# Kernel tuning notes

Hardware: AMD Instinct MI355X
Metric: run time of the kernel (lower is better)

The kernel has to match this reference:

```python
import jax, jax.numpy as jnp
import numpy as np

EPSILON = 0.1
SCALE = 10000.0

N = 16777216
G = 1024


def setup_inputs() -> dict:
    key = jax.random.key(0)
    k1, k2, k3 = jax.random.split(key, 3)
    pred = jax.random.normal(k1, (N,), dtype=jnp.float32)
    target = jax.random.normal(k2, (N,), dtype=jnp.float32)
    batch = jnp.sort(jax.random.randint(k3, (N,), 0, G).astype(jnp.int64))
    x = jnp.zeros((N,), dtype=jnp.float32)  # accepted by forward but unused
    return {"pred": pred, "target": target, "batch": batch, "x": x, "num_graphs": G}


def reference(pred, target, batch, x, num_graphs):
    # Per-node relative error
    rel = jnp.abs(pred - target) / (jnp.abs(target) + EPSILON)  # [N]
    # Fused per-graph mean via segment reduction (replaces python loop over graphs)
    sums = jax.ops.segment_sum(rel, batch, num_segments=num_graphs)           # [G]
    counts = jax.ops.segment_sum(jnp.ones_like(rel), batch, num_segments=num_graphs)  # [G]
    graph_means = sums / counts  # every segment nonempty w.h.p. for N >> G
    return jnp.mean(graph_means) * SCALE
```

## Files before the change

### kernel.cpp

```cpp
#include <hip/hip_runtime.h>


#define EPSILON_F 0.1f
#define SCALE_F 10000.0f

constexpr int BLOCK = 256;
constexpr int EPB = 8192;
constexpr int IT = EPB / (BLOCK * 4);

__device__ __forceinline__ int load_batch(const int* __restrict__ b32,
                                          long long idx, bool is64) {
  return b32[is64 ? (idx << 1) : idx];
}

__global__ __launch_bounds__(BLOCK)
void gre_seg(const float* __restrict__ pred, const float* __restrict__ target,
             const int* __restrict__ batch32, int n,
             float* __restrict__ sums, float* __restrict__ cnts) {
  const int tid = threadIdx.x;
  const long long s = (long long)blockIdx.x * EPB;
  long long e = s + EPB;
  if (e > n) e = n;

  const bool is64 = (batch32[n - 1] == 0);

  float r[IT][4];
  #pragma unroll
  for (int it = 0; it < IT; ++it) {
    long long i4 = s + (long long)(it * BLOCK + tid) * 4;
    if (i4 + 4 <= e) {
      float4 p4 = *reinterpret_cast<const float4*>(pred + i4);
      float4 t4 = *reinterpret_cast<const float4*>(target + i4);
      r[it][0] = fabsf(p4.x - t4.x) / (fabsf(t4.x) + EPSILON_F);
      r[it][1] = fabsf(p4.y - t4.y) / (fabsf(t4.y) + EPSILON_F);
      r[it][2] = fabsf(p4.z - t4.z) / (fabsf(t4.z) + EPSILON_F);
      r[it][3] = fabsf(p4.w - t4.w) / (fabsf(t4.w) + EPSILON_F);
    } else {
      #pragma unroll
      for (int j = 0; j < 4; ++j) {
        long long i = i4 + j;
        r[it][j] = (i < e)
            ? fabsf(pred[i] - target[i]) / (fabsf(target[i]) + EPSILON_F)
            : 0.f;
      }
    }
  }

  const int b0 = load_batch(batch32, s, is64);
  const int b1 = load_batch(batch32, e - 1, is64);

  float A = 0.f, B = 0.f;
  long long p = e;
  bool fast = true;

  if (b0 == b1) {
    #pragma unroll
    for (int it = 0; it < IT; ++it)
      #pragma unroll
      for (int j = 0; j < 4; ++j) A += r[it][j];
  } else if (b1 == b0 + 1) {
    long long lo = s, hi = e - 1;
    while (hi - lo > 1) {
      long long mid = (lo + hi) >> 1;
      if (load_batch(batch32, mid, is64) > b0) hi = mid; else lo = mid;
    }
    p = hi;
    #pragma unroll
    for (int it = 0; it < IT; ++it) {
      long long i4 = s + (long long)(it * BLOCK + tid) * 4;
      #pragma unroll
      for (int j = 0; j < 4; ++j) {
        if (i4 + j < p) A += r[it][j]; else B += r[it][j];
      }
    }
  } else {
    fast = false;
    #pragma unroll
    for (int it = 0; it < IT; ++it) {
      long long i4 = s + (long long)(it * BLOCK + tid) * 4;
      for (int j = 0; j < 4; ++j) {
        long long i = i4 + j;
        if (i < e) {
          int gi = load_batch(batch32, i, is64);
          atomicAdd(&sums[gi], r[it][j]);
          atomicAdd(&cnts[gi], 1.f);
        }
      }
    }
  }

  if (fast) {
    #pragma unroll
    for (int off = 32; off > 0; off >>= 1) {
      A += __shfl_down(A, off, 64);
      B += __shfl_down(B, off, 64);
    }
    if ((tid & 63) == 0) {
      atomicAdd(&sums[b0], A);
      if (b1 != b0) atomicAdd(&sums[b1], B);
    }
    if (tid == 0) {
      if (b0 == b1) {
        atomicAdd(&cnts[b0], (float)(e - s));
      } else {
        atomicAdd(&cnts[b0], (float)(p - s));
        atomicAdd(&cnts[b1], (float)(e - p));
      }
    }
  }
}

__global__ __launch_bounds__(64)
void gre_final(const float* __restrict__ sums, const float* __restrict__ cnts,
               float* __restrict__ out, int g) {
  const int tid = threadIdx.x;
  float v = 0.f;
  for (int i = tid; i < g; i += 64) v += sums[i] / cnts[i];
  #pragma unroll
  for (int off = 32; off > 0; off >>= 1) v += __shfl_down(v, off, 64);
  if (tid == 0) out[0] = (v / (float)g) * SCALE_F;
}

extern "C" void kernel_launch(void* const* d_in, const int* in_sizes, int n_in,
                              void* d_out, int out_size, void* d_ws, size_t ws_size,
                              hipStream_t stream) {
  const float* pred   = (const float*)d_in[0];
  const float* target = (const float*)d_in[1];
  const int*   batch  = (const int*)d_in[2];
  const int n = in_sizes[0];
  const int g = 1024;

  float* sums = (float*)d_ws;
  float* cnts = sums + g;
  hipMemsetAsync(d_ws, 0, 2 * g * sizeof(float), stream);

  const int nblocks = (n + EPB - 1) / EPB;
  gre_seg<<<nblocks, BLOCK, 0, stream>>>(pred, target, batch, n, sums, cnts);
  gre_final<<<1, 64, 0, stream>>>(sums, cnts, (float*)d_out, g);
}
```

Measured before the change: 224.0 us.

## Precompute segment starts by binary search and fuse final reduction into main kernel

A new small kernel binary-searches the sorted batch array for each graph's start offset. Per-graph counts then come from differences of those offsets instead of atomic count accumulation, and the split point inside two-segment blocks comes from the same table instead of a per-block search. The separate finalize kernel is replaced by a last-block-done pattern that uses an atomic counter and fences inside the main kernel. Register arrays are dropped in favour of streaming accumulation. This adds one launch for the starts kernel but removes the final launch and the count atomics.

```diff
diff --git a/kernel.cpp b/kernel.cpp
--- a/kernel.cpp
+++ b/kernel.cpp
@@ -7,6 +7,7 @@
 constexpr int BLOCK = 256;
 constexpr int EPB = 8192;
 constexpr int IT = EPB / (BLOCK * 4);
+constexpr int G_CONST = 1024;
 
 __device__ __forceinline__ int load_batch(const int* __restrict__ b32,
                                           long long idx, bool is64) {
@@ -14,111 +15,135 @@
 }
 
 __global__ __launch_bounds__(BLOCK)
-void gre_seg(const float* __restrict__ pred, const float* __restrict__ target,
-             const int* __restrict__ batch32, int n,
-             float* __restrict__ sums, float* __restrict__ cnts) {
+void gre_starts(const int* __restrict__ batch32, int n, int g,
+                int* __restrict__ starts) {
+  const int t = blockIdx.x * BLOCK + threadIdx.x;
+  if (t > g) return;
+  if (t == 0) { starts[0] = 0; return; }
+  if (t == g) { starts[g] = n; return; }
+  const bool is64 = (batch32[n - 1] == 0);
+  int lo = 0, hi = n;
+  while (lo < hi) {
+    int mid = (lo + hi) >> 1;
+    if (load_batch(batch32, mid, is64) < t) lo = mid + 1; else hi = mid;
+  }
+  starts[t] = lo;
+}
+
+__global__ __launch_bounds__(BLOCK)
+void gre_main(const float* __restrict__ pred, const float* __restrict__ target,
+              const int* __restrict__ batch32, int n, int g,
+              const int* __restrict__ starts, float* __restrict__ sums,
+              unsigned int* __restrict__ done, float* __restrict__ out) {
   const int tid = threadIdx.x;
   const long long s = (long long)blockIdx.x * EPB;
   long long e = s + EPB;
   if (e > n) e = n;
-
   const bool is64 = (batch32[n - 1] == 0);
-
-  float r[IT][4];
-  #pragma unroll
-  for (int it = 0; it < IT; ++it) {
-    long long i4 = s + (long long)(it * BLOCK + tid) * 4;
-    if (i4 + 4 <= e) {
-      float4 p4 = *reinterpret_cast<const float4*>(pred + i4);
-      float4 t4 = *reinterpret_cast<const float4*>(target + i4);
-      r[it][0] = fabsf(p4.x - t4.x) / (fabsf(t4.x) + EPSILON_F);
-      r[it][1] = fabsf(p4.y - t4.y) / (fabsf(t4.y) + EPSILON_F);
-      r[it][2] = fabsf(p4.z - t4.z) / (fabsf(t4.z) + EPSILON_F);
-      r[it][3] = fabsf(p4.w - t4.w) / (fabsf(t4.w) + EPSILON_F);
-    } else {
-      #pragma unroll
-      for (int j = 0; j < 4; ++j) {
-        long long i = i4 + j;
-        r[it][j] = (i < e)
-            ? fabsf(pred[i] - target[i]) / (fabsf(target[i]) + EPSILON_F)
-            : 0.f;
-      }
-    }
-  }
-
   const int b0 = load_batch(batch32, s, is64);
   const int b1 = load_batch(batch32, e - 1, is64);
 
   float A = 0.f, B = 0.f;
-  long long p = e;
-  bool fast = true;
 
-  if (b0 == b1) {
-    #pragma unroll
-    for (int it = 0; it < IT; ++it)
-      #pragma unroll
-      for (int j = 0; j < 4; ++j) A += r[it][j];
-  } else if (b1 == b0 + 1) {
-    long long lo = s, hi = e - 1;
-    while (hi - lo > 1) {
-      long long mid = (lo + hi) >> 1;
-      if (load_batch(batch32, mid, is64) > b0) hi = mid; else lo = mid;
-    }
-    p = hi;
+  if (b1 == b0) {
+    float Bx = 0.f, By = 0.f;
     #pragma unroll
     for (int it = 0; it < IT; ++it) {
       long long i4 = s + (long long)(it * BLOCK + tid) * 4;
-      #pragma unroll
-      for (int j = 0; j < 4; ++j) {
-        if (i4 + j < p) A += r[it][j]; else B += r[it][j];
+      if (i4 + 4 <= e) {
+        float4 pv = *reinterpret_cast<const float4*>(pred + i4);
+        float4 tv = *reinterpret_cast<const float4*>(target + i4);
+        Bx += fabsf(pv.x - tv.x) / (fabsf(tv.x) + EPSILON_F);
+        By += fabsf(pv.y - tv.y) / (fabsf(tv.y) + EPSILON_F);
+        Bx += fabsf(pv.z - tv.z) / (fabsf(tv.z) + EPSILON_F);
+        By += fabsf(pv.w - tv.w) / (fabsf(tv.w) + EPSILON_F);
+      } else {
+        for (int j = 0; j < 4; ++j) {
+          long long i = i4 + j;
+          if (i < e)
+            Bx += fabsf(pred[i] - target[i]) / (fabsf(target[i]) + EPSILON_F);
+        }
+      }
+    }
+    B = Bx + By;
+  } else if (b1 == b0 + 1) {
+    const long long p = (long long)starts[b1];
+    #pragma unroll
+    for (int it = 0; it < IT; ++it) {
+      long long i4 = s + (long long)(it * BLOCK + tid) * 4;
+      if (i4 + 4 <= e) {
+        float4 pv = *reinterpret_cast<const float4*>(pred + i4);
+        float4 tv = *reinterpret_cast<const float4*>(target + i4);
+        float r0 = fabsf(pv.x - tv.x) / (fabsf(tv.x) + EPSILON_F);
+        float r1 = fabsf(pv.y - tv.y) / (fabsf(tv.y) + EPSILON_F);
+        float r2 = fabsf(pv.z - tv.z) / (fabsf(tv.z) + EPSILON_F);
+        float r3 = fabsf(pv.w - tv.w) / (fabsf(tv.w) + EPSILON_F);
+        A += (i4 + 0 < p) ? r0 : 0.f;  B += (i4 + 0 < p) ? 0.f : r0;
+        A += (i4 + 1 < p) ? r1 : 0.f;  B += (i4 + 1 < p) ? 0.f : r1;
+        A += (i4 + 2 < p) ? r2 : 0.f;  B += (i4 + 2 < p) ? 0.f : r2;
+        A += (i4 + 3 < p) ? r3 : 0.f;  B += (i4 + 3 < p) ? 0.f : r3;
+      } else {
+        for (int j = 0; j < 4; ++j) {
+          long long i = i4 + j;
+          if (i < e) {
+            float r = fabsf(pred[i] - target[i]) / (fabsf(target[i]) + EPSILON_F);
+            if (i < p) A += r; else B += r;
+          }
+        }
       }
     }
   } else {
-    fast = false;
-    #pragma unroll
     for (int it = 0; it < IT; ++it) {
       long long i4 = s + (long long)(it * BLOCK + tid) * 4;
       for (int j = 0; j < 4; ++j) {
         long long i = i4 + j;
         if (i < e) {
           int gi = load_batch(batch32, i, is64);
-          atomicAdd(&sums[gi], r[it][j]);
-          atomicAdd(&cnts[gi], 1.f);
+          float r = fabsf(pred[i] - target[i]) / (fabsf(target[i]) + EPSILON_F);
+          atomicAdd(&sums[gi], r);
         }
       }
     }
   }
 
-  if (fast) {
+  #pragma unroll
+  for (int off = 32; off > 0; off >>= 1) {
+    A += __shfl_down(A, off, 64);
+    B += __shfl_down(B, off, 64);
+  }
+  if ((tid & 63) == 0) {
+    atomicAdd(&sums[b1], B);
+    if (b1 != b0) atomicAdd(&sums[b0], A);
+  }
+
+  __syncthreads();
+  __threadfence();
+  __shared__ unsigned int rank_s;
+  if (tid == 0)
+    rank_s = __hip_atomic_fetch_add(done, 1u, __ATOMIC_ACQ_REL,
+                                    __HIP_MEMORY_SCOPE_AGENT);
+  __syncthreads();
+  if (rank_s == gridDim.x - 1) {
+    __threadfence();
+    float v = 0.f;
+    for (int i = tid; i < g; i += BLOCK) {
+      float sv = __hip_atomic_load(&sums[i], __ATOMIC_RELAXED,
+                                   __HIP_MEMORY_SCOPE_AGENT);
+      int c = starts[i + 1] - starts[i];
+      v += sv / (float)c;
+    }
     #pragma unroll
-    for (int off = 32; off > 0; off >>= 1) {
-      A += __shfl_down(A, off, 64);
-      B += __shfl_down(B, off, 64);
-    }
-    if ((tid & 63) == 0) {
-      atomicAdd(&sums[b0], A);
-      if (b1 != b0) atomicAdd(&sums[b1], B);
-    }
+    for (int off = 32; off > 0; off >>= 1) v += __shfl_down(v, off, 64);
+    __shared__ float wsum[BLOCK / 64];
+    if ((tid & 63) == 0) wsum[tid >> 6] = v;
+    __syncthreads();
     if (tid == 0) {
-      if (b0 == b1) {
-        atomicAdd(&cnts[b0], (float)(e - s));
-      } else {
-        atomicAdd(&cnts[b0], (float)(p - s));
-        atomicAdd(&cnts[b1], (float)(e - p));
-      }
+      float t = 0.f;
+      #pragma unroll
+      for (int w = 0; w < BLOCK / 64; ++w) t += wsum[w];
+      out[0] = (t / (float)g) * SCALE_F;
     }
   }
-}
-
-__global__ __launch_bounds__(64)
-void gre_final(const float* __restrict__ sums, const float* __restrict__ cnts,
-               float* __restrict__ out, int g) {
-  const int tid = threadIdx.x;
-  float v = 0.f;
-  for (int i = tid; i < g; i += 64) v += sums[i] / cnts[i];
-  #pragma unroll
-  for (int off = 32; off > 0; off >>= 1) v += __shfl_down(v, off, 64);
-  if (tid == 0) out[0] = (v / (float)g) * SCALE_F;
 }
 
 extern "C" void kernel_launch(void* const* d_in, const int* in_sizes, int n_in,
@@ -128,13 +153,16 @@
   const float* target = (const float*)d_in[1];
   const int*   batch  = (const int*)d_in[2];
   const int n = in_sizes[0];
-  const int g = 1024;
+  const int g = G_CONST;
 
   float* sums = (float*)d_ws;
-  float* cnts = sums + g;
-  hipMemsetAsync(d_ws, 0, 2 * g * sizeof(float), stream);
+  int* starts = (int*)((char*)d_ws + 4096);
+  unsigned int* done = (unsigned int*)((char*)d_ws + 4096 + 1056 * 4);
+  hipMemsetAsync(d_ws, 0, 4096 + 1056 * 4 + 64, stream);
+
+  gre_starts<<<(g + BLOCK) / BLOCK, BLOCK, 0, stream>>>(batch, n, g, starts);
 
   const int nblocks = (n + EPB - 1) / EPB;
-  gre_seg<<<nblocks, BLOCK, 0, stream>>>(pred, target, batch, n, sums, cnts);
-  gre_final<<<1, 64, 0, stream>>>(sums, cnts, (float*)d_out, g);
+  gre_main<<<nblocks, BLOCK, 0, stream>>>(pred, target, batch, n, g, starts,
+                                          sums, done, (float*)d_out);
 }
```

Measured after the change: 513.2 us. 2.29x slower.
